# Kernel optimization log

Hardware: AMD Instinct MI355X
Metric: run time of the kernel (lower is better)

The kernel has to match this reference:

```python
import jax, jax.numpy as jnp
import numpy as np

N = 100000   # nodes
E = 1600000  # edges
F = 64       # input_features == output_features
BN_EPS = 1e-5


def _bn(x, gamma, beta):
    # torch BatchNorm1d (training mode): biased batch statistics
    mu = jnp.mean(x, axis=0)
    var = jnp.var(x, axis=0)
    return (x - mu) * jax.lax.rsqrt(var + BN_EPS) * gamma + beta


def setup_inputs() -> dict:
    key = jax.random.key(0)
    ks = jax.random.split(key, 16)
    s = 0.05
    inp = {
        'node_feats': jax.random.normal(ks[0], (N, F), jnp.float32),
        'edge_feats': jax.random.normal(ks[1], (E, F), jnp.float32),
        'src': jax.random.randint(ks[2], (E,), 0, N, jnp.int32),
        'dst': jax.random.randint(ks[3], (E,), 0, N, jnp.int32),
        # linear params: W [F_in, F_out], b [F_out]
        'W_src_gate': jax.random.normal(ks[4], (F, F), jnp.float32) * s,
        'b_src_gate': jnp.zeros((F,), jnp.float32),
        'W_dst_gate': jax.random.normal(ks[5], (F, F), jnp.float32) * s,
        'b_dst_gate': jnp.zeros((F,), jnp.float32),
        'W_edge_gate': jax.random.normal(ks[6], (F, F), jnp.float32) * s,
        'b_edge_gate': jnp.zeros((F,), jnp.float32),
        'W_src_update': jax.random.normal(ks[7], (F, F), jnp.float32) * s,
        'b_src_update': jnp.zeros((F,), jnp.float32),
        'W_dst_update': jax.random.normal(ks[8], (F, F), jnp.float32) * s,
        'b_dst_update': jnp.zeros((F,), jnp.float32),
        'bn_nodes_gamma': jnp.ones((F,), jnp.float32),
        'bn_nodes_beta': jnp.zeros((F,), jnp.float32),
        'bn_edges_gamma': jnp.ones((F,), jnp.float32),
        'bn_edges_beta': jnp.zeros((F,), jnp.float32),
    }
    return inp


def reference(node_feats, edge_feats, src, dst,
              W_src_gate, b_src_gate, W_dst_gate, b_dst_gate,
              W_edge_gate, b_edge_gate, W_src_update, b_src_update,
              W_dst_update, b_dst_update,
              bn_nodes_gamma, bn_nodes_beta, bn_edges_gamma, bn_edges_beta):
    # EdgeGatedGraphConv (arXiv:1711.07553), residual=True
    e_src = node_feats @ W_src_gate + b_src_gate          # [N,F]
    e_dst = node_feats @ W_dst_gate + b_dst_gate          # [N,F]
    # u_add_v gather + edge transform -> gate logits m [E,F]
    m = e_src[src] + e_dst[dst] + (edge_feats @ W_edge_gate + b_edge_gate)
    sigma = jax.nn.sigmoid(m)                             # [E,F]
    Bh = node_feats @ W_dst_update + b_dst_update         # [N,F]
    # u_mul_e message + scatter-sum to destination nodes
    sum_sigma_h = jax.ops.segment_sum(Bh[src] * sigma, dst, num_segments=node_feats.shape[0])
    sum_sigma = jax.ops.segment_sum(sigma, dst, num_segments=node_feats.shape[0])
    h = sum_sigma_h / (sum_sigma + 1e-6)                  # normalized aggregation
    x = node_feats @ W_src_update + b_src_update + h
    x = jax.nn.silu(_bn(x, bn_nodes_gamma, bn_nodes_beta))
    y = jax.nn.silu(_bn(m, bn_edges_gamma, bn_edges_beta))
    x = node_feats + x   # residual
    y = edge_feats + y   # residual
    return (x, y)
```

## Files before the change

### kernel.cpp

```cpp
#include <hip/hip_runtime.h>
#include <hip/hip_bf16.h>

typedef __attribute__((ext_vector_type(8))) __bf16 bf16x8;
typedef __attribute__((ext_vector_type(4))) float f32x4;

#define MFMA(a,b,c) __builtin_amdgcn_mfma_f32_16x16x32_bf16((a),(b),(c),0,0,0)

__device__ __forceinline__ bf16x8 cvt8(float4 a, float4 b){
  bf16x8 r;
  r[0]=(__bf16)a.x; r[1]=(__bf16)a.y; r[2]=(__bf16)a.z; r[3]=(__bf16)a.w;
  r[4]=(__bf16)b.x; r[5]=(__bf16)b.y; r[6]=(__bf16)b.z; r[7]=(__bf16)b.w;
  return r;
}

__global__ void setup_k(const float* __restrict__ W_sg, const float* __restrict__ W_dg,
                        const float* __restrict__ W_eg, const float* __restrict__ W_su,
                        const float* __restrict__ W_du,
                        bf16x8* __restrict__ Wq,
                        int4* __restrict__ zp, int nz4){
  if (blockIdx.x < 16){
    int tid = blockIdx.x*256 + threadIdx.x;
    if (tid >= 2560) return;
    int lane = tid & 63, g = lane>>4, c = lane&15;
    int frag = (tid>>6)&7, m = tid>>9;
    const float* Ws[5] = {W_eg, W_sg, W_dg, W_du, W_su};
    const float* W = Ws[m];
    int mt = frag>>1, kh = frag&1;
    bf16x8 v;
    #pragma unroll
    for (int j=0;j<8;j++) v[j] = (__bf16)W[(kh*32+g*8+j)*64 + mt*16 + c];
    Wq[tid] = v;
  } else {
    int i = (blockIdx.x-16)*256 + threadIdx.x, st = (gridDim.x-16)*256;
    for (; i<nz4; i+=st) zp[i] = make_int4(0,0,0,0);
  }
}

__global__ __launch_bounds__(256) void xform_hist_k(
    const float* __restrict__ nf, const bf16x8* __restrict__ Wq,
    __bf16* __restrict__ es16, __bf16* __restrict__ ed16,
    __bf16* __restrict__ bh16, float* __restrict__ A_src, int ntiles, int nxf,
    const int* __restrict__ dst, int* __restrict__ cnt, int E)
{
  if ((int)blockIdx.x < nxf){
    int lane = threadIdx.x & 63;
    int gw = blockIdx.x*4 + (threadIdx.x>>6);
    if (gw >= ntiles) return;
    int g = lane>>4, c = lane&15;
    long base = (long)gw*16;
    const float* rp = nf + (base + c)*64 + g*8;
    float4 a0 = *(const float4*)rp,      a1 = *(const float4*)(rp+4);
    float4 a2 = *(const float4*)(rp+32), a3 = *(const float4*)(rp+36);
    bf16x8 B0 = cvt8(a0,a1), B1 = cvt8(a2,a3);
    __bf16* outs[3] = {es16, ed16, bh16};
    const int mats[3] = {1,2,3};
    #pragma unroll
    for (int i=0;i<3;i++){
      #pragma unroll
      for (int mt=0;mt<4;mt++){
        f32x4 am = {0.f,0.f,0.f,0.f};
        am = MFMA(Wq[(mats[i]*8+mt*2+0)*64+lane], B0, am);
        am = MFMA(Wq[(mats[i]*8+mt*2+1)*64+lane], B1, am);
        union { __bf16 h[4]; uint2 u; } pk;
        #pragma unroll
        for (int e=0;e<4;e++) pk.h[e] = (__bf16)am[e];
        *(uint2*)(outs[i] + (base+c)*64 + mt*16 + 4*g) = pk.u;
      }
    }
    #pragma unroll
    for (int mt=0;mt<4;mt++){
      f32x4 am = {0.f,0.f,0.f,0.f};
      am = MFMA(Wq[(4*8+mt*2+0)*64+lane], B0, am);
      am = MFMA(Wq[(4*8+mt*2+1)*64+lane], B1, am);
      *(float4*)(A_src + (base+c)*64 + mt*16 + 4*g) =
        make_float4(am[0],am[1],am[2],am[3]);
    }
  } else {
    int nb = gridDim.x - nxf;
    int i = (blockIdx.x-nxf)*256 + threadIdx.x, st = nb*256;
    for (; i<E; i+=st) atomicAdd(&cnt[dst[i]], 1);
  }
}

__global__ __launch_bounds__(1024) void scan_k(const int* __restrict__ cnt,
                                               int* __restrict__ row, int Nn){
  __shared__ int part[1024];
  int t = threadIdx.x;
  int C = (Nn + 1023) >> 10;
  int lo = t*C;
  int hi = lo + C; if (hi > Nn) hi = Nn;
  int s = 0;
  for (int i=lo; i<hi; i++) s += cnt[i];
  part[t] = s;
  __syncthreads();
  for (int off=1; off<1024; off<<=1){
    int v = part[t];
    int u = (t>=off) ? part[t-off] : 0;
    __syncthreads();
    part[t] = v + u;
    __syncthreads();
  }
  int excl = (t==0) ? 0 : part[t-1];
  for (int i=lo; i<hi; i++){ row[i] = excl; excl += cnt[i]; }
  if (t==1023) row[Nn] = excl;
}

#define NFILL 1024
__global__ __launch_bounds__(256) void fillA_k(
    const int* __restrict__ src, const int* __restrict__ dst,
    const int* __restrict__ rowp, int* __restrict__ cnt2,
    int2* __restrict__ pairs, int E,
    const float* __restrict__ ef,
    const __bf16* __restrict__ es16, const __bf16* __restrict__ ed16,
    const float* __restrict__ b_sg, const float* __restrict__ b_dg,
    const float* __restrict__ b_eg,
    const bf16x8* __restrict__ Wq,
    __bf16* __restrict__ m16, int ntiles)
{
  __shared__ bf16x8 wl[8*64];
  if (blockIdx.x < NFILL){
    int i = blockIdx.x*256 + threadIdx.x, st = NFILL*256;
    for (; i<E; i+=st){
      int d = dst[i];
      int pos = rowp[d] + atomicAdd(&cnt2[d], 1);
      pairs[pos] = make_int2(i, src[i]);
    }
    return;
  }
  {
    int t = threadIdx.x;
    #pragma unroll
    for (int i=0;i<2;i++) wl[i*256+t] = Wq[i*256+t];
  }
  __syncthreads();
  int lane = threadIdx.x & 63, g = lane>>4, c = lane&15;
  bf16x8 I0, I1;
  #pragma unroll
  for (int j=0;j<8;j++){
    I0[j] = (g*8+j == c)      ? (__bf16)1.0f : (__bf16)0.0f;
    I1[j] = (g*8+j == 16 + c) ? (__bf16)1.0f : (__bf16)0.0f;
  }
  int gw = (blockIdx.x-NFILL)*4 + (threadIdx.x>>6);
  int nw = (gridDim.x-NFILL)*4;
  float bias2[4][4];
  #pragma unroll
  for (int mt=0;mt<4;mt++)
    #pragma unroll
    for (int e=0;e<4;e++){
      int f = mt*16 + 4*g + e;
      bias2[mt][e] = b_sg[f] + b_dg[f] + b_eg[f];
    }
  if (gw >= ntiles) return;
  int sc = src[(long)gw*16 + c], dc = dst[(long)gw*16 + c];
  for (int tt=gw; tt<ntiles; tt+=nw){
    long base = (long)tt*16;
    int tn = tt + nw;
    int sn = sc, dn = dc;
    if (tn < ntiles){ sn = src[(long)tn*16 + c]; dn = dst[(long)tn*16 + c]; }
    const float* rpe = ef + (base+c)*64 + g*8;
    float4 e0=*(const float4*)rpe,      e1=*(const float4*)(rpe+4);
    float4 e2=*(const float4*)(rpe+32), e3=*(const float4*)(rpe+36);
    bf16x8 BS0 = *(const bf16x8*)(es16 + (long)sc*64 + g*8);
    bf16x8 BS1 = *(const bf16x8*)(es16 + (long)sc*64 + 32 + g*8);
    bf16x8 BD0 = *(const bf16x8*)(ed16 + (long)dc*64 + g*8);
    bf16x8 BD1 = *(const bf16x8*)(ed16 + (long)dc*64 + 32 + g*8);
    bf16x8 BE0=cvt8(e0,e1), BE1=cvt8(e2,e3);
    #pragma unroll
    for (int mt=0;mt<4;mt++){
      bf16x8 Is = (mt&1) ? I1 : I0;
      f32x4 am = {0.f,0.f,0.f,0.f};
      am = MFMA(wl[(mt*2+0)*64+lane], BE0, am);
      am = MFMA(wl[(mt*2+1)*64+lane], BE1, am);
      am = MFMA(Is, (mt>>1) ? BS1 : BS0, am);
      am = MFMA(Is, (mt>>1) ? BD1 : BD0, am);
      union { __bf16 h[4]; uint2 u; } pk;
      #pragma unroll
      for (int e=0;e<4;e++) pk.h[e] = (__bf16)(am[e] + bias2[mt][e]);
      *(uint2*)(m16 + (base+c)*64 + mt*16 + 4*g) = pk.u;
    }
    sc = sn; dc = dn;
  }
}

__global__ __launch_bounds__(256) void phaseB(
    const __bf16* __restrict__ m16, const int2* __restrict__ pairs,
    const __bf16* __restrict__ bh16, const int* __restrict__ rowp,
    const float* __restrict__ b_du, const float* __restrict__ b_su,
    float* __restrict__ A_src,
    float* __restrict__ est, float* __restrict__ nst, int Nn)
{
  __shared__ float sst[256];
  sst[threadIdx.x] = 0.f;
  __syncthreads();
  int lane = threadIdx.x & 63, w = threadIdx.x>>6;
  float bdu = b_du[lane], bsu = b_su[lane];
  int chunk = (Nn + gridDim.x - 1)/gridDim.x;
  int n0 = blockIdx.x*chunk;
  int n1 = n0 + chunk; if (n1 > Nn) n1 = Nn;
  float e1=0.f, e2=0.f, p1=0.f, p2=0.f;
  for (int n=n0+w; n<n1; n+=4){
    int r0 = rowp[n], r1 = rowp[n+1];
    float ssum=0.f, bsum=0.f;
    int r = r0;
    for (; r+8 <= r1; r+=8){
      int2 q[8];
      #pragma unroll
      for (int j=0;j<8;j++) q[j] = pairs[r+j];
      float mv[8], bh[8];
      #pragma unroll
      for (int j=0;j<8;j++) mv[j] = (float)m16[(long)q[j].x*64 + lane];
      #pragma unroll
      for (int j=0;j<8;j++) bh[j] = (float)bh16[(long)q[j].y*64 + lane] + bdu;
      #pragma unroll
      for (int j=0;j<8;j++){
        float sg = 1.f/(1.f+__expf(-mv[j]));
        ssum += sg; bsum += bh[j]*sg;
        e1 += mv[j]; e2 += mv[j]*mv[j];
      }
    }
    for (; r < r1; ++r){
      int2 q0 = pairs[r];
      float mv0 = (float)m16[(long)q0.x*64 + lane];
      float bh0 = (float)bh16[(long)q0.y*64 + lane] + bdu;
      float sg0 = 1.f/(1.f+__expf(-mv0));
      ssum += sg0; bsum += bh0*sg0;
      e1 += mv0;   e2 += mv0*mv0;
    }
    long xi = (long)n*64 + lane;
    float xp = A_src[xi] + bsu + bsum/(ssum+1e-6f);
    A_src[xi] = xp;
    p1 += xp; p2 += xp*xp;
  }
  atomicAdd(&sst[lane],     e1);
  atomicAdd(&sst[64+lane],  e2);
  atomicAdd(&sst[128+lane], p1);
  atomicAdd(&sst[192+lane], p2);
  __syncthreads();
  int t = threadIdx.x;
  if (t < 128) atomicAdd(&est[t], sst[t]);
  else         atomicAdd(&nst[t-128], sst[t]);
}

#define NNF 1024
__global__ __launch_bounds__(256) void finals_k(
    const float* __restrict__ nf, const float* __restrict__ xpre,
    const float* __restrict__ nst, const float* __restrict__ gn,
    const float* __restrict__ btn, float* __restrict__ xo, int Nn,
    const __bf16* __restrict__ m16, const float* __restrict__ ef,
    const float* __restrict__ est, const float* __restrict__ ge,
    const float* __restrict__ bte, float* __restrict__ y, float invE, long E)
{
  if (blockIdx.x < NNF){
    long tid = (long)blockIdx.x*256 + threadIdx.x;
    long stride = (long)NNF*256;
    int col = (int)(tid & 63);
    float invN = 1.f/(float)Nn;
    float mu = nst[col]*invN;
    float var = nst[64+col]*invN - mu*mu;
    float rs = rsqrtf(var + 1e-5f);
    float aa = gn[col]*rs;
    float bb = btn[col] - mu*aa;
    long total = (long)Nn*64;
    for (long i=tid; i<total; i+=stride){
      float z = xpre[i]*aa + bb;
      xo[i] = nf[i] + z/(1.f+__expf(-z));
    }
  } else {
    int oct = threadIdx.x & 7;
    float aa[8], bb[8];
    #pragma unroll
    for (int j=0;j<8;j++){
      int col = oct*8 + j;
      float mu = est[col]*invE;
      float var = est[64+col]*invE - mu*mu;
      float rs = rsqrtf(var + 1e-5f);
      float ga = ge[col]*rs;
      aa[j] = ga; bb[j] = bte[col] - mu*ga;
    }
    long tid = (long)(blockIdx.x-NNF)*256 + threadIdx.x;
    long pstep = ((long)(gridDim.x-NNF)*256) >> 3;
    for (long p = tid>>3; p < E; p += pstep){
      bf16x8 mv = *(const bf16x8*)&m16[p*64 + oct*8];
      const float* rp = ef + p*64 + oct*8;
      float4 f0 = *(const float4*)rp, f1 = *(const float4*)(rp+4);
      float o[8];
      #pragma unroll
      for (int j=0;j<8;j++){
        float z = aa[j]*(float)mv[j] + bb[j];
        float ev = (j<4) ? ((const float*)&f0)[j] : ((const float*)&f1)[j-4];
        o[j] = ev + z/(1.f+__expf(-z));
      }
      float* yp = y + p*64 + oct*8;
      *(float4*)yp     = make_float4(o[0],o[1],o[2],o[3]);
      *(float4*)(yp+4) = make_float4(o[4],o[5],o[6],o[7]);
    }
  }
}

extern "C" void kernel_launch(void* const* d_in, const int* in_sizes, int n_in,
                              void* d_out, int out_size, void* d_ws, size_t ws_size,
                              hipStream_t stream){
  const float* nf  = (const float*)d_in[0];
  const float* ef  = (const float*)d_in[1];
  const int*   src = (const int*)d_in[2];
  const int*   dst = (const int*)d_in[3];
  const float* W_sg=(const float*)d_in[4];  const float* b_sg=(const float*)d_in[5];
  const float* W_dg=(const float*)d_in[6];  const float* b_dg=(const float*)d_in[7];
  const float* W_eg=(const float*)d_in[8];  const float* b_eg=(const float*)d_in[9];
  const float* W_su=(const float*)d_in[10]; const float* b_su=(const float*)d_in[11];
  const float* W_du=(const float*)d_in[12]; const float* b_du=(const float*)d_in[13];
  const float* gn=(const float*)d_in[14];   const float* btn=(const float*)d_in[15];
  const float* ge=(const float*)d_in[16];   const float* bte=(const float*)d_in[17];

  int Nn = in_sizes[0]/64;
  int Ee = in_sizes[2];
  size_t Nf = (size_t)Nn*64;
  size_t Es = (size_t)Ee;

  float* ws    = (float*)d_ws;
  float* A_src = ws;
  __bf16* es16 = (__bf16*)(ws + Nf);
  __bf16* ed16 = (__bf16*)(ws + Nf + Nf/2);
  __bf16* bh16 = (__bf16*)(ws + 2*Nf);
  __bf16* m16  = (__bf16*)(ws + 2*Nf + Nf/2);
  int2*  pairs = (int2*)(ws + 2*Nf + Nf/2 + 32*Es);
  int*   cnt   = (int*)(pairs + Es);
  int*   cnt2  = cnt + Nn;
  float* est   = (float*)(cnt2 + Nn);
  float* nst   = est + 128;
  int*   rowp  = (int*)(nst + 128);
  size_t woff  = 2*Nf + Nf/2 + 32*Es + 2*Es + 2*(size_t)Nn + 256 + (size_t)Nn + 1;
  woff = (woff + 15) & ~(size_t)15;
  bf16x8* Wq   = (bf16x8*)(ws + woff);

  float* xo = (float*)d_out;
  float* yo = xo + Nf;

  int nz4 = (int)((2*(size_t)Nn + 256) >> 2);
  setup_k<<<272,256,0,stream>>>(W_sg,W_dg,W_eg,W_su,W_du,Wq,(int4*)cnt,nz4);

  int ntn = Nn/16;
  int nxf = (ntn+3)/4;
  xform_hist_k<<<nxf+2048,256,0,stream>>>(nf,Wq,es16,ed16,bh16,A_src,ntn,nxf,
                                          dst,cnt,Ee);
  scan_k<<<1,1024,0,stream>>>(cnt,rowp,Nn);
  int nte = Ee/16;
  fillA_k<<<NFILL+4096,256,0,stream>>>(src,dst,rowp,cnt2,pairs,Ee,
                                       ef,es16,ed16,b_sg,b_dg,b_eg,Wq,m16,nte);
  phaseB<<<4096,256,0,stream>>>(m16,pairs,bh16,rowp,b_du,b_su,A_src,est,nst,Nn);
  finals_k<<<NNF+4096,256,0,stream>>>(nf,A_src,nst,gn,btn,xo,Nn,
                                      m16,ef,est,ge,bte,yo,
                                      1.f/(float)Ee,(long)Ee);
}
```

Baseline: 902.5 us.

## Prefetch next edge tile operands and stage m16 stores through LDS

The edge-gate loop in fillA_k now loads the next tile's edge features and gathered src/dst bf16 rows one iteration ahead, with indices prefetched two tiles ahead. This hides gather latency behind the MFMA work. Output gate values are first written to a per-wave XOR-swizzled LDS buffer, then stored as coalesced 16-byte writes of contiguous rows instead of scattered 8-byte stores. The cost is more registers and extra LDS traffic, which may lower occupancy.

```diff
diff --git a/kernel.cpp b/kernel.cpp
--- a/kernel.cpp
+++ b/kernel.cpp
@@ -105,6 +105,26 @@
   if (t==1023) row[Nn] = excl;
 }
 
+struct T2 {
+  float4 e0,e1,e2,e3;
+  bf16x8 bs0,bs1,bd0,bd1;
+};
+
+__device__ __forceinline__ T2 ld_t2(const float* __restrict__ ef,
+                                    const __bf16* __restrict__ es16,
+                                    const __bf16* __restrict__ ed16,
+                                    long base, int c, int g, int sc, int dc){
+  T2 t;
+  const float* rpe = ef + (base+c)*64 + g*8;
+  t.e0=*(const float4*)rpe;      t.e1=*(const float4*)(rpe+4);
+  t.e2=*(const float4*)(rpe+32); t.e3=*(const float4*)(rpe+36);
+  t.bs0 = *(const bf16x8*)(es16 + (long)sc*64 + g*8);
+  t.bs1 = *(const bf16x8*)(es16 + (long)sc*64 + 32 + g*8);
+  t.bd0 = *(const bf16x8*)(ed16 + (long)dc*64 + g*8);
+  t.bd1 = *(const bf16x8*)(ed16 + (long)dc*64 + 32 + g*8);
+  return t;
+}
+
 #define NFILL 1024
 __global__ __launch_bounds__(256) void fillA_k(
     const int* __restrict__ src, const int* __restrict__ dst,
@@ -118,6 +138,7 @@
     __bf16* __restrict__ m16, int ntiles)
 {
   __shared__ bf16x8 wl[8*64];
+  __shared__ uint2 mst[4][256];
   if (blockIdx.x < NFILL){
     int i = blockIdx.x*256 + threadIdx.x, st = NFILL*256;
     for (; i<E; i+=st){
@@ -134,13 +155,14 @@
   }
   __syncthreads();
   int lane = threadIdx.x & 63, g = lane>>4, c = lane&15;
+  int wv = threadIdx.x>>6;
   bf16x8 I0, I1;
   #pragma unroll
   for (int j=0;j<8;j++){
     I0[j] = (g*8+j == c)      ? (__bf16)1.0f : (__bf16)0.0f;
     I1[j] = (g*8+j == 16 + c) ? (__bf16)1.0f : (__bf16)0.0f;
   }
-  int gw = (blockIdx.x-NFILL)*4 + (threadIdx.x>>6);
+  int gw = (blockIdx.x-NFILL)*4 + wv;
   int nw = (gridDim.x-NFILL)*4;
   float bias2[4][4];
   #pragma unroll
@@ -152,33 +174,42 @@
     }
   if (gw >= ntiles) return;
   int sc = src[(long)gw*16 + c], dc = dst[(long)gw*16 + c];
+  T2 cur = ld_t2(ef, es16, ed16, (long)gw*16, c, g, sc, dc);
+  int t1i = gw + nw;
+  int sn = sc, dn = dc;
+  if (t1i < ntiles){ sn = src[(long)t1i*16 + c]; dn = dst[(long)t1i*16 + c]; }
+  int r_o = lane>>3;
+  int u0_o = (lane&7)*2;
   for (int tt=gw; tt<ntiles; tt+=nw){
-    long base = (long)tt*16;
-    int tn = tt + nw;
-    int sn = sc, dn = dc;
-    if (tn < ntiles){ sn = src[(long)tn*16 + c]; dn = dst[(long)tn*16 + c]; }
-    const float* rpe = ef + (base+c)*64 + g*8;
-    float4 e0=*(const float4*)rpe,      e1=*(const float4*)(rpe+4);
-    float4 e2=*(const float4*)(rpe+32), e3=*(const float4*)(rpe+36);
-    bf16x8 BS0 = *(const bf16x8*)(es16 + (long)sc*64 + g*8);
-    bf16x8 BS1 = *(const bf16x8*)(es16 + (long)sc*64 + 32 + g*8);
-    bf16x8 BD0 = *(const bf16x8*)(ed16 + (long)dc*64 + g*8);
-    bf16x8 BD1 = *(const bf16x8*)(ed16 + (long)dc*64 + 32 + g*8);
-    bf16x8 BE0=cvt8(e0,e1), BE1=cvt8(e2,e3);
+    int t1 = tt + nw;
+    T2 nxt;
+    if (t1 < ntiles) nxt = ld_t2(ef, es16, ed16, (long)t1*16, c, g, sn, dn);
+    int t2 = t1 + nw;
+    if (t2 < ntiles){ sn = src[(long)t2*16 + c]; dn = dst[(long)t2*16 + c]; }
+    bf16x8 BE0=cvt8(cur.e0,cur.e1), BE1=cvt8(cur.e2,cur.e3);
     #pragma unroll
     for (int mt=0;mt<4;mt++){
       bf16x8 Is = (mt&1) ? I1 : I0;
       f32x4 am = {0.f,0.f,0.f,0.f};
       am = MFMA(wl[(mt*2+0)*64+lane], BE0, am);
       am = MFMA(wl[(mt*2+1)*64+lane], BE1, am);
-      am = MFMA(Is, (mt>>1) ? BS1 : BS0, am);
-      am = MFMA(Is, (mt>>1) ? BD1 : BD0, am);
+      am = MFMA(Is, (mt>>1) ? cur.bs1 : cur.bs0, am);
+      am = MFMA(Is, (mt>>1) ? cur.bd1 : cur.bd0, am);
       union { __bf16 h[4]; uint2 u; } pk;
       #pragma unroll
       for (int e=0;e<4;e++) pk.h[e] = (__bf16)(am[e] + bias2[mt][e]);
-      *(uint2*)(m16 + (base+c)*64 + mt*16 + 4*g) = pk.u;
-    }
-    sc = sn; dc = dn;
+      int u = mt*4 + g;
+      mst[wv][c*16 + (u^c)] = pk.u;
+    }
+    char* tb = (char*)m16 + (size_t)tt*16*128;
+    #pragma unroll
+    for (int k=0;k<2;k++){
+      int r = k*8 + r_o;
+      uint2 a = mst[wv][r*16 + ( u0_o      ^ r)];
+      uint2 b = mst[wv][r*16 + ((u0_o + 1) ^ r)];
+      *(uint4*)(tb + k*1024 + lane*16) = make_uint4(a.x,a.y,b.x,b.y);
+    }
+    cur = nxt;
   }
 }
 
```

Result: faster. 864.2 us (-4.2%).
